# Optimization experiments

Hardware: AMD Instinct MI355X
Metric: run time of the kernel (lower is better)

The kernel has to match this reference:

```python
import math
import jax, jax.numpy as jnp
from jax import lax
import numpy as np

SCORE_THR = 0.5
IOU_THR = 0.7
MIN_SIZE = 1.0
BBOX_CLIP = math.log(1000.0 / 16.0)

FEAT_SIZES = [100, 50, 25, 13, 7]
STRIDES = [8, 16, 32, 64, 128]
RATIOS = (0.5, 1.0, 2.0)
C = 256
A = 3
N = 2


def _make_priors(fs, stride):
    base = stride * 4.0
    ys, xs = np.meshgrid(np.arange(fs), np.arange(fs), indexing='ij')
    cx = (xs + 0.5) * stride
    cy = (ys + 0.5) * stride
    pri = []
    for r in RATIOS:
        w = base / np.sqrt(r)
        h = base * np.sqrt(r)
        pri.append(np.stack([cx - w / 2, cy - h / 2, cx + w / 2, cy + h / 2], axis=-1))
    pri = np.stack(pri, axis=2)  # (fs, fs, A, 4): H,W,A order matches permute/reshape
    return jnp.asarray(pri.reshape(-1, 4), dtype=jnp.float32)


def setup_inputs():
    key = jax.random.key(0)
    ks = jax.random.split(key, 8)
    inp = {}
    for i, fs in enumerate(FEAT_SIZES):
        inp[f'fmap{i}'] = jax.random.normal(jax.random.fold_in(ks[0], i), (N, C, fs, fs), dtype=jnp.float32)
        inp[f'priors{i}'] = _make_priors(fs, STRIDES[i])
    sc = 0.02
    inp['conv_w'] = jax.random.normal(ks[1], (C, C, 3, 3), jnp.float32) * sc
    inp['conv_b'] = jnp.zeros((C,), jnp.float32)
    inp['log_w'] = jax.random.normal(ks[2], (A, C, 1, 1), jnp.float32) * sc
    inp['log_b'] = jnp.zeros((A,), jnp.float32)
    inp['reg_w'] = jax.random.normal(ks[3], (A * 4, C, 1, 1), jnp.float32) * sc
    inp['reg_b'] = jnp.zeros((A * 4,), jnp.float32)
    inp['imsizes'] = jnp.full((N, 2), 800, dtype=jnp.int32)  # (h, w) per image
    inp['lvtop'] = 500
    inp['imtop'] = 100
    return inp


def _conv(x, w, b, pad):
    y = lax.conv_general_dilated(x, w, (1, 1), pad, dimension_numbers=('NCHW', 'OIHW', 'NCHW'))
    return y + b[None, :, None, None]


def _decode(reg, pri):
    pw = pri[..., 2] - pri[..., 0]
    ph = pri[..., 3] - pri[..., 1]
    pcx = pri[..., 0] + 0.5 * pw
    pcy = pri[..., 1] + 0.5 * ph
    dx, dy = reg[..., 0], reg[..., 1]
    dw = jnp.minimum(reg[..., 2], BBOX_CLIP)
    dh = jnp.minimum(reg[..., 3], BBOX_CLIP)
    cx = dx * pw + pcx
    cy = dy * ph + pcy
    w = jnp.exp(dw) * pw
    h = jnp.exp(dh) * ph
    return jnp.stack([cx - 0.5 * w, cy - 0.5 * h, cx + 0.5 * w, cy + 0.5 * h], axis=-1)


def _head(x, priors, conv_w, conv_b, log_w, log_b, reg_w, reg_b, lvtop):
    n = x.shape[0]
    h = jax.nn.relu(_conv(x, conv_w, conv_b, 'SAME'))
    reg = _conv(h, reg_w, reg_b, 'VALID').transpose(0, 2, 3, 1).reshape(n, -1, 4)
    log = _conv(h, log_w, log_b, 'VALID').transpose(0, 2, 3, 1).reshape(n, -1)
    k = min(lvtop, log.shape[1])
    vals, top = lax.top_k(log, k)                           # (n, k)
    reg = jnp.take_along_axis(reg, top[..., None], axis=1)  # (n, k, 4)
    pri = priors[top]                                       # (n, k, 4)
    return _decode(reg, pri), vals, k


def _box_iou(a, b):
    area_a = (a[:, 2] - a[:, 0]) * (a[:, 3] - a[:, 1])
    area_b = (b[:, 2] - b[:, 0]) * (b[:, 3] - b[:, 1])
    lt = jnp.maximum(a[:, None, :2], b[None, :, :2])
    rb = jnp.minimum(a[:, None, 2:], b[None, :, 2:])
    wh = jnp.clip(rb - lt, 0.0)
    inter = wh[..., 0] * wh[..., 1]
    return inter / (area_a[:, None] + area_b[None, :] - inter + 1e-9)


def _forward(fmaps, priors, conv_w, conv_b, log_w, log_b, reg_w, reg_b, imsizes, lvtop, imtop):
    tups = [_head(x, p, conv_w, conv_b, log_w, log_b, reg_w, reg_b, lvtop)
            for x, p in zip(fmaps, priors)]
    boxes = jnp.concatenate([t[0] for t in tups], axis=1)                 # (n, D, 4)
    obj = jax.nn.sigmoid(jnp.concatenate([t[1] for t in tups], axis=1))   # (n, D)
    lvlen = jnp.asarray([t[2] for t in tups])
    n, D = obj.shape
    boxes = boxes.reshape(-1, 4)
    obj = obj.reshape(-1)
    K = n * D
    imidx = jnp.arange(K) // D
    valid = obj >= SCORE_THR                                # score filter (masked, not nonzero)
    hw = imsizes[imidx].astype(jnp.float32)                 # (K, 2) = (h, w)
    x1 = jnp.clip(boxes[:, 0], 0.0, hw[:, 1])
    y1 = jnp.clip(boxes[:, 1], 0.0, hw[:, 0])
    x2 = jnp.clip(boxes[:, 2], 0.0, hw[:, 1])
    y2 = jnp.clip(boxes[:, 3], 0.0, hw[:, 0])
    boxes = jnp.stack([x1, y1, x2, y2], axis=-1)
    valid &= (x2 - x1 >= MIN_SIZE) & (y2 - y1 >= MIN_SIZE)  # remove_small
    lvidx = jnp.searchsorted(jnp.cumsum(lvlen), jnp.arange(K) % D, side='right')
    groups = imidx * 10 + lvidx
    scores = jnp.where(valid, obj, -jnp.inf)
    order = jnp.argsort(-scores)                            # global score order; groups gate suppression
    b, g, v, ii = boxes[order], groups[order], valid[order], imidx[order]
    iou = _box_iou(b, b)                                    # (K, K)
    ar = jnp.arange(K)
    def body(i, keep):
        sup = (iou[i] > IOU_THR) & (g == g[i]) & (ar > i)
        return jnp.where(keep[i], keep & ~sup, keep)
    keep = lax.fori_loop(0, K, body, v)                     # greedy batched NMS
    def select(i):
        m = keep & (ii == i)
        sel = jnp.argsort(~m)[:imtop]                       # stable: kept boxes in score order
        val = m[sel]
        bx = jnp.where(val[:, None], b[sel], 0.0)
        ix = jnp.where(val, i, -1)
        return bx, ix
    bx, ix = jax.vmap(select)(jnp.arange(n))
    return bx.reshape(n * imtop, 4), ix.reshape(n * imtop)


def reference(fmap0, fmap1, fmap2, fmap3, fmap4, priors0, priors1, priors2, priors3, priors4,
              conv_w, conv_b, log_w, log_b, reg_w, reg_b, imsizes, lvtop, imtop):
    return _forward([fmap0, fmap1, fmap2, fmap3, fmap4],
                    [priors0, priors1, priors2, priors3, priors4],
                    conv_w, conv_b, log_w, log_b, reg_w, reg_b, imsizes, lvtop, imtop)
```

## Files before the change

kernel.cpp:

```cpp
#include <hip/hip_runtime.h>
#include <math.h>


#define N_IMG 2
#define C_CH  256
#define D_PER 2147
#define K_TOT 4294
#define K_PAD 8192

__constant__ int c_Ml[5]     = {30000, 7500, 1875, 507, 147};
__constant__ int c_kl[5]     = {500, 500, 500, 500, 147};
__constant__ int c_lvoff[5]  = {0, 500, 1000, 1500, 2000};
__constant__ int c_logoff[5] = {0, 60000, 75000, 78750, 79764};
__constant__ int c_regoff[5] = {0, 240000, 300000, 315000, 319056};
__constant__ int c_fs[5]     = {100, 50, 25, 13, 7};
__constant__ int c_npt[5]    = {13, 7, 4, 2, 1};
__constant__ int c_E[5]      = {10000, 2500, 625, 169, 49};
__constant__ int c_cumbl[6]  = {0, 1352, 1744, 1872, 1904, 1912};
__constant__ int c_hcum[6]   = {0, 157, 197, 207, 210, 211};
__constant__ size_t c_hoff[5] = {0, 5120000, 6400000, 6720000, 6806528};

__global__ void transpose_w_kernel(const float* __restrict__ w,
                                   double* __restrict__ wT2) {
  int i = blockIdx.x * 256 + threadIdx.x;
  if (i >= 589824) return;
  int q = i % 4608;
  int slab = i / 4608;
  int cobi = slab >> 5, ch = slab & 31;
  int ci = q / 576;
  int rem = q % 576;
  int tap = rem / 64, co = rem & 63;
  wT2[i] = (double)w[(size_t)(cobi * 64 + co) * 2304 + (ch * 8 + ci) * 9 + tap];
}

template <typename T>
__global__ __launch_bounds__(256) void conv_fused_kernel(
    const float* __restrict__ x0, const float* __restrict__ x1,
    const float* __restrict__ x2, const float* __restrict__ x3,
    const float* __restrict__ x4, const double* __restrict__ wT2,
    const float* __restrict__ bias, T* __restrict__ h) {
  __shared__ double s_in[8][120];
  __shared__ double s_w[4608];
  int tid = threadIdx.x;
  int bid = blockIdx.x;
  int l = 0;
  while (bid >= c_cumbl[l + 1]) ++l;
  int r = bid - c_cumbl[l];
  int fs = c_fs[l], npt = c_npt[l];
  int tiles = npt * npt;
  int tile = r % tiles;
  int cn = r / tiles;
  int cobi = cn & 3, n = cn >> 2;
  int ptx = tile % npt, pty = tile / npt;
  int px0 = ptx * 8, py0 = pty * 8;
  int E = fs * fs;
  const float* xl;
  switch (l) {
    case 0: xl = x0; break;
    case 1: xl = x1; break;
    case 2: xl = x2; break;
    case 3: xl = x3; break;
    default: xl = x4; break;
  }
  const float* xn = xl + (size_t)n * C_CH * E;
  T* hl = h + c_hoff[l];

  int tpx = tid & 15, tco = tid >> 4;
  int prow = tpx >> 1, pcol0 = (tpx & 1) * 4;

  double acc[4][4];
#pragma unroll
  for (int i = 0; i < 4; i++)
#pragma unroll
    for (int j = 0; j < 4; j++) acc[i][j] = 0.0;

  for (int ch = 0; ch < 32; ++ch) {
    for (int idx = tid; idx < 800; idx += 256) {
      int ci = idx / 100, rr2 = idx % 100;
      int hy = rr2 / 10, hx = rr2 % 10;
      int gy = py0 - 1 + hy, gx = px0 - 1 + hx;
      float v = 0.f;
      if (gy >= 0 && gy < fs && gx >= 0 && gx < fs)
        v = xn[(size_t)(ch * 8 + ci) * E + gy * fs + gx];
      s_in[ci][hy * 12 + hx] = (double)v;
    }
    {
      const double2* src =
          (const double2*)(wT2 + (size_t)(cobi * 32 + ch) * 4608);
      double2* dst = (double2*)s_w;
#pragma unroll
      for (int k = 0; k < 9; k++) {
        int idx = tid + k * 256;
        if (idx < 2304) dst[idx] = src[idx];
      }
    }
    __syncthreads();
#pragma unroll
    for (int ci = 0; ci < 8; ++ci) {
      const double* inp = &s_in[ci][0];
      const double* wpb = &s_w[ci * 576];
#pragma unroll
      for (int ky = 0; ky < 3; ++ky) {
        const double* ip = inp + (prow + ky) * 12 + pcol0;
        double2 a0 = *(const double2*)ip;
        double2 a1 = *(const double2*)(ip + 2);
        double2 a2 = *(const double2*)(ip + 4);
        double d6[6];
        d6[0] = a0.x; d6[1] = a0.y; d6[2] = a1.x;
        d6[3] = a1.y; d6[4] = a2.x; d6[5] = a2.y;
#pragma unroll
        for (int kx = 0; kx < 3; ++kx) {
          const double* wp = wpb + (ky * 3 + kx) * 64 + tco * 4;
          double2 wA = *(const double2*)wp;
          double2 wB = *(const double2*)(wp + 2);
          double w0 = wA.x, w1 = wA.y, w2 = wB.x, w3 = wB.y;
#pragma unroll
          for (int pj = 0; pj < 4; pj++) {
            double iv = d6[pj + kx];
            acc[0][pj] = fma(w0, iv, acc[0][pj]);
            acc[1][pj] = fma(w1, iv, acc[1][pj]);
            acc[2][pj] = fma(w2, iv, acc[2][pj]);
            acc[3][pj] = fma(w3, iv, acc[3][pj]);
          }
        }
      }
    }
    __syncthreads();
  }

  int gy = py0 + prow;
  if (gy < fs) {
#pragma unroll
    for (int coi = 0; coi < 4; ++coi) {
      int co = cobi * 64 + tco * 4 + coi;
      double bb = (double)bias[co];
#pragma unroll
      for (int pj = 0; pj < 4; pj++) {
        int gx = px0 + pcol0 + pj;
        if (gx < fs) {
          double v = acc[coi][pj] + bb;
          hl[((size_t)n * C_CH + co) * E + gy * fs + gx] = (T)fmax(v, 0.0);
        }
      }
    }
  }
}

template <typename T>
__global__ __launch_bounds__(256) void heads_fused_kernel(
    const T* __restrict__ h, const float* __restrict__ logw,
    const float* __restrict__ logb, const float* __restrict__ regw,
    const float* __restrict__ regb, double* __restrict__ logits,
    double* __restrict__ regs) {
  __shared__ float s_wh[256][16];
  __shared__ double s_red[4][15][64];
  int tid = threadIdx.x;
  int n = blockIdx.y;
  int cidx = blockIdx.x;
  int l = 0;
  while (cidx >= c_hcum[l + 1]) ++l;
  int chunk = cidx - c_hcum[l];
  int E = c_E[l];
  int px0 = chunk * 64;
  const T* hl = h + c_hoff[l];
  double* logits_l = logits + c_logoff[l];
  double* regs_l = regs + c_regoff[l];

  for (int idx = tid; idx < 4096; idx += 256) {
    int c = idx >> 4, j = idx & 15;
    float v = 0.f;
    if (j < 3) v = logw[j * 256 + c];
    else if (j < 15) v = regw[(j - 3) * 256 + c];
    s_wh[c][j] = v;
  }
  __syncthreads();

  int p = tid & 63, c4 = tid >> 6;
  int pix = px0 + p;
  bool act = pix < E;
  double acc[15];
#pragma unroll
  for (int j = 0; j < 15; j++) acc[j] = 0.0;
  if (act) {
    const T* hp = hl + ((size_t)n * C_CH + c4 * 64) * E + pix;
    for (int cc = 0; cc < 64; ++cc) {
      double hv = (double)hp[(size_t)cc * E];
      const float* wr = &s_wh[c4 * 64 + cc][0];
#pragma unroll
      for (int j = 0; j < 15; j++)
        acc[j] = fma((double)wr[j], hv, acc[j]);
    }
  }
#pragma unroll
  for (int j = 0; j < 15; j++) s_red[c4][j][p] = acc[j];
  __syncthreads();
  if (act) {
    int M = E * 3;
    for (int j = c4; j < 15; j += 4) {
      double v = s_red[0][j][p] + s_red[1][j][p] + s_red[2][j][p] +
                 s_red[3][j][p];
      if (j < 3) {
        logits_l[(size_t)n * M + pix * 3 + j] = v + (double)logb[j];
      } else {
        int rj = j - 3, a = rj >> 2, coord = rj & 3;
        regs_l[((size_t)n * M + pix * 3 + a) * 4 + coord] =
            v + (double)regb[rj];
      }
    }
  }
}

__device__ __forceinline__ unsigned long long d2key(double v) {
  unsigned long long ub = (unsigned long long)__double_as_longlong(v);
  return (ub >> 63) ? ~ub : (ub | 0x8000000000000000ull);
}

#define TK_CH 30
__global__ __launch_bounds__(1024) void topk_kernel(
    const double* __restrict__ logits, int* __restrict__ cand_anchor) {
  int bid = blockIdx.x;
  int n = bid / 5, l = bid % 5;
  int M = c_Ml[l], k = c_kl[l];
  const double* lg = logits + c_logoff[l] + (size_t)n * M;
  int tid = threadIdx.x;
  __shared__ int histw[16][256];
  __shared__ int hist[256];
  __shared__ unsigned long long s_prefix;
  __shared__ int s_r;
  if (tid == 0) { s_prefix = 0ull; s_r = k; }

  int chunk = (M + 1023) >> 10;
  int i0 = tid * chunk, i1 = min(M, i0 + chunk);
  int cnt = i1 - i0;
  if (cnt < 0) cnt = 0;
  unsigned long long kv[TK_CH];
#pragma unroll
  for (int q = 0; q < TK_CH; q++)
    if (q < cnt) kv[q] = d2key(lg[i0 + q]);
  int wid = tid >> 6;
  __syncthreads();

  for (int pass = 0; pass < 8; ++pass) {
    int shift = 56 - pass * 8;
    for (int i = tid; i < 4096; i += 1024) ((int*)histw)[i] = 0;
    __syncthreads();
    unsigned long long pfx = s_prefix;
    int rr = s_r;
#pragma unroll
    for (int q = 0; q < TK_CH; q++) {
      if (q < cnt) {
        unsigned long long u = kv[q];
        if (pass == 0 || (u >> (shift + 8)) == pfx)
          atomicAdd(&histw[wid][(int)((u >> shift) & 255ull)], 1);
      }
    }
    __syncthreads();
    if (tid < 256) {
      int s = 0;
#pragma unroll
      for (int w = 0; w < 16; w++) s += histw[w][tid];
      hist[tid] = s;
    }
    __syncthreads();
    if (tid == 0) {
      int s = 0, beta = 0;
      for (int b = 255; b >= 0; --b) {
        if (s + hist[b] >= rr) { beta = b; break; }
        s += hist[b];
      }
      s_prefix = (pfx << 8) | (unsigned long long)beta;
      s_r = rr - s;
    }
    __syncthreads();
  }
  unsigned long long T = s_prefix;
  int need = s_r;
  int cgt = 0, ceq = 0;
#pragma unroll
  for (int q = 0; q < TK_CH; q++) {
    if (q < cnt) {
      cgt += (kv[q] > T);
      ceq += (kv[q] == T);
    }
  }
  __shared__ int sgt[1024], seq[1024];
  sgt[tid] = cgt;
  seq[tid] = ceq;
  __syncthreads();
  for (int o = 1; o < 1024; o <<= 1) {
    int a = (tid >= o) ? sgt[tid - o] : 0;
    int b2 = (tid >= o) ? seq[tid - o] : 0;
    __syncthreads();
    sgt[tid] += a;
    seq[tid] += b2;
    __syncthreads();
  }
  int gt_total = sgt[1023];
  int pg = sgt[tid] - cgt, pe = seq[tid] - ceq;
  int base = n * D_PER + c_lvoff[l];
#pragma unroll
  for (int q = 0; q < TK_CH; q++) {
    if (q < cnt) {
      unsigned long long u = kv[q];
      if (u > T) {
        cand_anchor[base + (pg++)] = i0 + q;
      } else if (u == T) {
        if (pe < need) cand_anchor[base + gt_total + pe] = i0 + q;
        pe++;
      }
    }
  }
}

__global__ __launch_bounds__(256) void decode_kernel(
    const int* __restrict__ cand_anchor, const double* __restrict__ logits,
    const double* __restrict__ regs, const float* __restrict__ p0,
    const float* __restrict__ p1, const float* __restrict__ p2,
    const float* __restrict__ p3, const float* __restrict__ p4,
    const int* __restrict__ imsizes, double* __restrict__ cand_score,
    double* __restrict__ cand_box, int* __restrict__ cand_group,
    int* __restrict__ cand_valid) {
  int s = blockIdx.x * 256 + threadIdx.x;
  if (s >= K_TOT) return;
  int n = s / D_PER;
  int rr = s % D_PER;
  int l = (rr < 2000) ? (rr / 500) : 4;
  int aidx = cand_anchor[s];
  int M = c_Ml[l];
  const float* pp;
  switch (l) {
    case 0: pp = p0; break;
    case 1: pp = p1; break;
    case 2: pp = p2; break;
    case 3: pp = p3; break;
    default: pp = p4; break;
  }
  double lv = logits[c_logoff[l] + (size_t)n * M + aidx];
  double obj = 1.0 / (1.0 + exp(-lv));
  const double* rp = regs + c_regoff[l] + ((size_t)n * M + aidx) * 4;
  const float* pr = pp + (size_t)aidx * 4;
  double px1 = pr[0], py1 = pr[1], px2 = pr[2], py2 = pr[3];
  double pw = px2 - px1, ph = py2 - py1;
  double pcx = px1 + 0.5 * pw, pcy = py1 + 0.5 * ph;
  const double BCLIP = 4.1351665567423560;
  double dx = rp[0], dy = rp[1];
  double dw = fmin(rp[2], BCLIP), dh = fmin(rp[3], BCLIP);
  double cx = dx * pw + pcx, cy = dy * ph + pcy;
  double w = exp(dw) * pw, hh = exp(dh) * ph;
  double x1 = cx - 0.5 * w, y1 = cy - 0.5 * hh;
  double x2 = cx + 0.5 * w, y2 = cy + 0.5 * hh;
  double imh = (double)imsizes[n * 2 + 0], imw = (double)imsizes[n * 2 + 1];
  x1 = fmin(fmax(x1, 0.0), imw);
  x2 = fmin(fmax(x2, 0.0), imw);
  y1 = fmin(fmax(y1, 0.0), imh);
  y2 = fmin(fmax(y2, 0.0), imh);
  bool valid = (obj >= 0.5) && ((x2 - x1) >= 1.0) && ((y2 - y1) >= 1.0);
  cand_box[(size_t)s * 4 + 0] = x1;
  cand_box[(size_t)s * 4 + 1] = y1;
  cand_box[(size_t)s * 4 + 2] = x2;
  cand_box[(size_t)s * 4 + 3] = y2;
  cand_score[s] = valid ? obj : -(double)INFINITY;
  cand_group[s] = n * 5 + l;
  cand_valid[s] = valid ? 1 : 0;
}

__global__ __launch_bounds__(1024) void sort_kernel(
    const double* __restrict__ cand_score, int* __restrict__ order) {
  __shared__ unsigned long long key[K_PAD];
  int tid = threadIdx.x;
  for (int i = tid; i < K_PAD; i += 1024) {
    unsigned long long kk = 0ull;
    if (i < K_TOT) {
      unsigned long long u = d2key(cand_score[i]);
      kk = (u & ~0x1FFFull) | (unsigned long long)i;
    }
    key[i] = kk;
  }
  __syncthreads();
  for (int k = 2; k <= K_PAD; k <<= 1) {
    for (int j = k >> 1; j > 0; j >>= 1) {
      for (int i = tid; i < K_PAD; i += 1024) {
        int ixj = i ^ j;
        if (ixj > i) {
          unsigned long long a = key[i], b = key[ixj];
          bool sw = ((i & k) == 0) ? (a < b) : (a > b);
          if (sw) { key[i] = b; key[ixj] = a; }
        }
      }
      __syncthreads();
    }
  }
  for (int i = tid; i < K_TOT; i += 1024)
    order[i] = (int)(key[i] & 0x1FFFull);
}

__global__ __launch_bounds__(256) void gather_kernel(
    const int* __restrict__ order, const double* __restrict__ cand_box,
    const int* __restrict__ cand_group, const int* __restrict__ cand_valid,
    double* __restrict__ box_s, int* __restrict__ grp_s,
    int* __restrict__ img_s, int* __restrict__ valid_s,
    int* __restrict__ keep_s) {
  int i = blockIdx.x * 256 + threadIdx.x;
  if (i >= K_TOT) return;
  int s = order[i];
#pragma unroll
  for (int q = 0; q < 4; q++)
    box_s[(size_t)i * 4 + q] = cand_box[(size_t)s * 4 + q];
  int g = cand_group[s];
  grp_s[i] = g;
  img_s[i] = g / 5;
  valid_s[i] = cand_valid[s];
  keep_s[i] = 0;
}

#define MAXM 512
__global__ __launch_bounds__(256) void nms_kernel(
    const double* __restrict__ box_s, const int* __restrict__ grp_s,
    const int* __restrict__ valid_s, int* __restrict__ keep_s) {
  int g = blockIdx.x;
  int tid = threadIdx.x;
  __shared__ int cnt[256];
  __shared__ int mem[MAXM];
  __shared__ double bx[MAXM][4];
  __shared__ unsigned long long mask[MAXM][8];
  const int chunk = (K_TOT + 255) / 256;
  int i0 = tid * chunk, i1 = min(K_TOT, i0 + chunk);
  int c = 0;
  for (int i = i0; i < i1; ++i) c += (grp_s[i] == g && valid_s[i]);
  cnt[tid] = c;
  __syncthreads();
  for (int o = 1; o < 256; o <<= 1) {
    int v = (tid >= o) ? cnt[tid - o] : 0;
    __syncthreads();
    cnt[tid] += v;
    __syncthreads();
  }
  int off = cnt[tid] - c;
  int m = cnt[255];
  for (int i = i0; i < i1; ++i)
    if (grp_s[i] == g && valid_s[i]) mem[off++] = i;
  __syncthreads();
  for (int t = tid; t < m; t += 256) {
    int i = mem[t];
#pragma unroll
    for (int q = 0; q < 4; q++) bx[t][q] = box_s[(size_t)i * 4 + q];
  }
  __syncthreads();
  for (int i = tid; i < m; i += 256) {
    unsigned long long row[8] = {0, 0, 0, 0, 0, 0, 0, 0};
    double ax1 = bx[i][0], ay1 = bx[i][1], ax2 = bx[i][2], ay2 = bx[i][3];
    double areaA = (ax2 - ax1) * (ay2 - ay1);
    for (int j = i + 1; j < m; ++j) {
      double bx1 = bx[j][0], by1 = bx[j][1], bx2 = bx[j][2], by2 = bx[j][3];
      double areaB = (bx2 - bx1) * (by2 - by1);
      double lx = fmax(ax1, bx1), ly = fmax(ay1, by1);
      double rx = fmin(ax2, bx2), ry = fmin(ay2, by2);
      double iw = fmax(rx - lx, 0.0), ih = fmax(ry - ly, 0.0);
      double inter = iw * ih;
      double iou = inter / (areaA + areaB - inter + 1e-9);
      if (iou > 0.7) row[j >> 6] |= (1ull << (j & 63));
    }
#pragma unroll
    for (int w2 = 0; w2 < 8; ++w2) mask[i][w2] = row[w2];
  }
  __syncthreads();
  if (tid == 0) {
    unsigned long long remv[8] = {0, 0, 0, 0, 0, 0, 0, 0};
    for (int i = 0; i < m; ++i) {
      if (!((remv[i >> 6] >> (i & 63)) & 1ull)) {
        keep_s[mem[i]] = 1;
#pragma unroll
        for (int w2 = 0; w2 < 8; ++w2) remv[w2] |= mask[i][w2];
      }
    }
  }
}

__global__ __launch_bounds__(256) void select_kernel(
    const double* __restrict__ box_s, const int* __restrict__ img_s,
    const int* __restrict__ keep_s, float* __restrict__ out) {
  int n = blockIdx.x;
  int tid = threadIdx.x;
  __shared__ int cnt[256];
  const int chunk = (K_TOT + 255) / 256;
  int i0 = tid * chunk, i1 = min(K_TOT, i0 + chunk);
  int c = 0;
  for (int i = i0; i < i1; ++i) c += (keep_s[i] && img_s[i] == n);
  cnt[tid] = c;
  __syncthreads();
  for (int o = 1; o < 256; o <<= 1) {
    int v = (tid >= o) ? cnt[tid - o] : 0;
    __syncthreads();
    cnt[tid] += v;
    __syncthreads();
  }
  int pos = cnt[tid] - c;
  int total = cnt[255];
  for (int i = i0; i < i1; ++i) {
    if (keep_s[i] && img_s[i] == n) {
      if (pos < 100) {
#pragma unroll
        for (int q = 0; q < 4; q++)
          out[(n * 100 + pos) * 4 + q] = (float)box_s[(size_t)i * 4 + q];
        out[800 + n * 100 + pos] = (float)n;
      }
      pos++;
    }
  }
  for (int p = total + tid; p < 100; p += 256) {
#pragma unroll
    for (int q = 0; q < 4; q++) out[(n * 100 + p) * 4 + q] = 0.0f;
    out[800 + n * 100 + p] = -1.0f;
  }
}

extern "C" void kernel_launch(void* const* d_in, const int* in_sizes, int n_in,
                              void* d_out, int out_size, void* d_ws,
                              size_t ws_size, hipStream_t stream) {
  (void)in_sizes; (void)n_in; (void)out_size;
  const float* fmap[5];
  const float* priors[5];
  for (int l = 0; l < 5; l++) {
    fmap[l] = (const float*)d_in[2 * l];
    priors[l] = (const float*)d_in[2 * l + 1];
  }
  const float* conv_w = (const float*)d_in[10];
  const float* conv_b = (const float*)d_in[11];
  const float* log_w = (const float*)d_in[12];
  const float* log_b = (const float*)d_in[13];
  const float* reg_w = (const float*)d_in[14];
  const float* reg_b = (const float*)d_in[15];
  const int* imsizes = (const int*)d_in[16];
  float* out = (float*)d_out;

  bool f64h = ws_size >= (size_t)66000000;

  char* base = (char*)d_ws;
  size_t off = 0;
  auto alloc = [&](size_t bytes) -> void* {
    off = (off + 255) & ~(size_t)255;
    void* p = base + off;
    off += bytes;
    return p;
  };
  double* wT2 = (double*)alloc(589824ull * 8);
  void* hraw = alloc(6831616ull * (f64h ? 8 : 4));
  double* logits = (double*)alloc(80058ull * 8);
  double* regs = (double*)alloc(320232ull * 8);
  int* cand_anchor = (int*)alloc(K_TOT * 4);
  double* cand_score = (double*)alloc(K_TOT * 8);
  double* cand_box = (double*)alloc((size_t)K_TOT * 4 * 8);
  int* cand_group = (int*)alloc(K_TOT * 4);
  int* cand_valid = (int*)alloc(K_TOT * 4);
  int* order = (int*)alloc(K_TOT * 4);
  double* box_s = (double*)alloc((size_t)K_TOT * 4 * 8);
  int* grp_s = (int*)alloc(K_TOT * 4);
  int* img_s = (int*)alloc(K_TOT * 4);
  int* valid_s = (int*)alloc(K_TOT * 4);
  int* keep_s = (int*)alloc(K_TOT * 4);

  transpose_w_kernel<<<2304, 256, 0, stream>>>(conv_w, wT2);

  if (f64h) {
    conv_fused_kernel<double><<<1912, 256, 0, stream>>>(
        fmap[0], fmap[1], fmap[2], fmap[3], fmap[4], wT2, conv_b,
        (double*)hraw);
    heads_fused_kernel<double><<<dim3(211, 2), 256, 0, stream>>>(
        (double*)hraw, log_w, log_b, reg_w, reg_b, logits, regs);
  } else {
    conv_fused_kernel<float><<<1912, 256, 0, stream>>>(
        fmap[0], fmap[1], fmap[2], fmap[3], fmap[4], wT2, conv_b,
        (float*)hraw);
    heads_fused_kernel<float><<<dim3(211, 2), 256, 0, stream>>>(
        (float*)hraw, log_w, log_b, reg_w, reg_b, logits, regs);
  }
  topk_kernel<<<10, 1024, 0, stream>>>(logits, cand_anchor);
  decode_kernel<<<(K_TOT + 255) / 256, 256, 0, stream>>>(
      cand_anchor, logits, regs, priors[0], priors[1], priors[2], priors[3],
      priors[4], imsizes, cand_score, cand_box, cand_group, cand_valid);
  sort_kernel<<<1, 1024, 0, stream>>>(cand_score, order);
  gather_kernel<<<(K_TOT + 255) / 256, 256, 0, stream>>>(
      order, cand_box, cand_group, cand_valid, box_s, grp_s, img_s, valid_s,
      keep_s);
  nms_kernel<<<10, 256, 0, stream>>>(box_s, grp_s, valid_s, keep_s);
  select_kernel<<<2, 256, 0, stream>>>(box_s, img_s, keep_s, out);
}
```

Before: 1.239 ms.

## Restructure conv to wave-uniform weight loads and fuse topk/decode, sort/gather

The conv kernel drops the shared-memory weight tile. Each wave now owns 16 output channels and reads weights directly from global memory with wave-uniform addresses, and each lane computes one pixel. Input staging indices are precomputed once, and block IDs are swizzled across the XCDs. Separately, topk is fused with decode through a shared selection list, and sort is fused with gather, which removes two launches and the intermediate buffers. The risks are reduced per-thread register reuse in the conv (one pixel per thread), more global/scalar load traffic, and dependence on the weight fetches being cached.

```diff
diff --git a/kernel.cpp b/kernel.cpp
--- a/kernel.cpp
+++ b/kernel.cpp
@@ -7,6 +7,8 @@
 #define D_PER 2147
 #define K_TOT 4294
 #define K_PAD 8192
+#define CONV_BLOCKS 1912
+#define CPX 239
 
 __constant__ int c_Ml[5]     = {30000, 7500, 1875, 507, 147};
 __constant__ int c_kl[5]     = {500, 500, 500, 500, 147};
@@ -30,7 +32,8 @@
   int ci = q / 576;
   int rem = q % 576;
   int tap = rem / 64, co = rem & 63;
-  wT2[i] = (double)w[(size_t)(cobi * 64 + co) * 2304 + (ch * 8 + ci) * 9 + tap];
+  wT2[i] =
+      (double)w[(size_t)(cobi * 64 + co) * 2304 + (ch * 8 + ci) * 9 + tap];
 }
 
 template <typename T>
@@ -39,10 +42,9 @@
     const float* __restrict__ x2, const float* __restrict__ x3,
     const float* __restrict__ x4, const double* __restrict__ wT2,
     const float* __restrict__ bias, T* __restrict__ h) {
-  __shared__ double s_in[8][120];
-  __shared__ double s_w[4608];
+  __shared__ double s_in[8 * 120];
   int tid = threadIdx.x;
-  int bid = blockIdx.x;
+  int bid = (blockIdx.x & 7) * CPX + (blockIdx.x >> 3);
   int l = 0;
   while (bid >= c_cumbl[l + 1]) ++l;
   int r = bid - c_cumbl[l];
@@ -65,83 +67,72 @@
   const float* xn = xl + (size_t)n * C_CH * E;
   T* hl = h + c_hoff[l];
 
-  int tpx = tid & 15, tco = tid >> 4;
-  int prow = tpx >> 1, pcol0 = (tpx & 1) * 4;
-
-  double acc[4][4];
-#pragma unroll
-  for (int i = 0; i < 4; i++)
-#pragma unroll
-    for (int j = 0; j < 4; j++) acc[i][j] = 0.0;
-
-  for (int ch = 0; ch < 32; ++ch) {
-    for (int idx = tid; idx < 800; idx += 256) {
+  int lane = tid & 63;
+  int wvu = __builtin_amdgcn_readfirstlane(tid >> 6);
+  int prow = lane >> 3, pcol = lane & 7;
+
+  int in_dst[4], in_src[4];
+#pragma unroll
+  for (int it = 0; it < 4; ++it) {
+    int idx = tid + it * 256;
+    in_dst[it] = -1;
+    in_src[it] = -1;
+    if (idx < 800) {
       int ci = idx / 100, rr2 = idx % 100;
       int hy = rr2 / 10, hx = rr2 % 10;
       int gy = py0 - 1 + hy, gx = px0 - 1 + hx;
-      float v = 0.f;
+      in_dst[it] = ci * 120 + hy * 12 + hx;
       if (gy >= 0 && gy < fs && gx >= 0 && gx < fs)
-        v = xn[(size_t)(ch * 8 + ci) * E + gy * fs + gx];
-      s_in[ci][hy * 12 + hx] = (double)v;
-    }
-    {
-      const double2* src =
-          (const double2*)(wT2 + (size_t)(cobi * 32 + ch) * 4608);
-      double2* dst = (double2*)s_w;
-#pragma unroll
-      for (int k = 0; k < 9; k++) {
-        int idx = tid + k * 256;
-        if (idx < 2304) dst[idx] = src[idx];
-      }
-    }
-    __syncthreads();
+        in_src[it] = ci * E + gy * fs + gx;
+    }
+  }
+
+  double acc[16];
+#pragma unroll
+  for (int c = 0; c < 16; ++c) acc[c] = 0.0;
+
+  const double* __restrict__ wbase =
+      wT2 + (size_t)(cobi * 32) * 4608 + wvu * 16;
+
+  for (int ch = 0; ch < 32; ++ch) {
+    const float* xc = xn + (size_t)(ch * 8) * E;
+#pragma unroll
+    for (int it = 0; it < 4; ++it) {
+      if (in_dst[it] >= 0)
+        s_in[in_dst[it]] = (in_src[it] >= 0) ? (double)xc[in_src[it]] : 0.0;
+    }
+    __syncthreads();
+    const double* __restrict__ wch = wbase + (size_t)ch * 4608;
 #pragma unroll
     for (int ci = 0; ci < 8; ++ci) {
-      const double* inp = &s_in[ci][0];
-      const double* wpb = &s_w[ci * 576];
+      const double* inp = &s_in[ci * 120];
 #pragma unroll
       for (int ky = 0; ky < 3; ++ky) {
-        const double* ip = inp + (prow + ky) * 12 + pcol0;
-        double2 a0 = *(const double2*)ip;
-        double2 a1 = *(const double2*)(ip + 2);
-        double2 a2 = *(const double2*)(ip + 4);
-        double d6[6];
-        d6[0] = a0.x; d6[1] = a0.y; d6[2] = a1.x;
-        d6[3] = a1.y; d6[4] = a2.x; d6[5] = a2.y;
+        const double* ip = inp + (prow + ky) * 12 + pcol;
+        double iv[3];
+        iv[0] = ip[0];
+        iv[1] = ip[1];
+        iv[2] = ip[2];
 #pragma unroll
         for (int kx = 0; kx < 3; ++kx) {
-          const double* wp = wpb + (ky * 3 + kx) * 64 + tco * 4;
-          double2 wA = *(const double2*)wp;
-          double2 wB = *(const double2*)(wp + 2);
-          double w0 = wA.x, w1 = wA.y, w2 = wB.x, w3 = wB.y;
-#pragma unroll
-          for (int pj = 0; pj < 4; pj++) {
-            double iv = d6[pj + kx];
-            acc[0][pj] = fma(w0, iv, acc[0][pj]);
-            acc[1][pj] = fma(w1, iv, acc[1][pj]);
-            acc[2][pj] = fma(w2, iv, acc[2][pj]);
-            acc[3][pj] = fma(w3, iv, acc[3][pj]);
-          }
+          const double* __restrict__ wk = wch + (ci * 9 + ky * 3 + kx) * 64;
+          double ivx = iv[kx];
+#pragma unroll
+          for (int c = 0; c < 16; ++c)
+            acc[c] = fma(wk[c], ivx, acc[c]);
         }
       }
     }
     __syncthreads();
   }
 
-  int gy = py0 + prow;
-  if (gy < fs) {
-#pragma unroll
-    for (int coi = 0; coi < 4; ++coi) {
-      int co = cobi * 64 + tco * 4 + coi;
-      double bb = (double)bias[co];
-#pragma unroll
-      for (int pj = 0; pj < 4; pj++) {
-        int gx = px0 + pcol0 + pj;
-        if (gx < fs) {
-          double v = acc[coi][pj] + bb;
-          hl[((size_t)n * C_CH + co) * E + gy * fs + gx] = (T)fmax(v, 0.0);
-        }
-      }
+  int gy = py0 + prow, gx = px0 + pcol;
+  if (gy < fs && gx < fs) {
+#pragma unroll
+    for (int c = 0; c < 16; ++c) {
+      int co = cobi * 64 + wvu * 16 + c;
+      double v = acc[c] + (double)bias[co];
+      hl[((size_t)n * C_CH + co) * E + gy * fs + gx] = (T)fmax(v, 0.0);
     }
   }
 }
@@ -216,8 +207,13 @@
 }
 
 #define TK_CH 30
-__global__ __launch_bounds__(1024) void topk_kernel(
-    const double* __restrict__ logits, int* __restrict__ cand_anchor) {
+__global__ __launch_bounds__(1024) void topk_decode_kernel(
+    const double* __restrict__ logits, const double* __restrict__ regs,
+    const float* __restrict__ p0, const float* __restrict__ p1,
+    const float* __restrict__ p2, const float* __restrict__ p3,
+    const float* __restrict__ p4, const int* __restrict__ imsizes,
+    double* __restrict__ cand_score, double* __restrict__ cand_box,
+    int* __restrict__ cand_group, int* __restrict__ cand_valid) {
   int bid = blockIdx.x;
   int n = bid / 5, l = bid % 5;
   int M = c_Ml[l], k = c_kl[l];
@@ -225,6 +221,7 @@
   int tid = threadIdx.x;
   __shared__ int histw[16][256];
   __shared__ int hist[256];
+  __shared__ int s_sel[512];
   __shared__ unsigned long long s_prefix;
   __shared__ int s_r;
   if (tid == 0) { s_prefix = 0ull; s_r = k; }
@@ -297,36 +294,20 @@
   }
   int gt_total = sgt[1023];
   int pg = sgt[tid] - cgt, pe = seq[tid] - ceq;
-  int base = n * D_PER + c_lvoff[l];
 #pragma unroll
   for (int q = 0; q < TK_CH; q++) {
     if (q < cnt) {
       unsigned long long u = kv[q];
       if (u > T) {
-        cand_anchor[base + (pg++)] = i0 + q;
+        s_sel[pg++] = i0 + q;
       } else if (u == T) {
-        if (pe < need) cand_anchor[base + gt_total + pe] = i0 + q;
+        if (pe < need) s_sel[gt_total + pe] = i0 + q;
         pe++;
       }
     }
   }
-}
-
-__global__ __launch_bounds__(256) void decode_kernel(
-    const int* __restrict__ cand_anchor, const double* __restrict__ logits,
-    const double* __restrict__ regs, const float* __restrict__ p0,
-    const float* __restrict__ p1, const float* __restrict__ p2,
-    const float* __restrict__ p3, const float* __restrict__ p4,
-    const int* __restrict__ imsizes, double* __restrict__ cand_score,
-    double* __restrict__ cand_box, int* __restrict__ cand_group,
-    int* __restrict__ cand_valid) {
-  int s = blockIdx.x * 256 + threadIdx.x;
-  if (s >= K_TOT) return;
-  int n = s / D_PER;
-  int rr = s % D_PER;
-  int l = (rr < 2000) ? (rr / 500) : 4;
-  int aidx = cand_anchor[s];
-  int M = c_Ml[l];
+  __syncthreads();
+
   const float* pp;
   switch (l) {
     case 0: pp = p0; break;
@@ -335,37 +316,46 @@
     case 3: pp = p3; break;
     default: pp = p4; break;
   }
-  double lv = logits[c_logoff[l] + (size_t)n * M + aidx];
-  double obj = 1.0 / (1.0 + exp(-lv));
-  const double* rp = regs + c_regoff[l] + ((size_t)n * M + aidx) * 4;
-  const float* pr = pp + (size_t)aidx * 4;
-  double px1 = pr[0], py1 = pr[1], px2 = pr[2], py2 = pr[3];
-  double pw = px2 - px1, ph = py2 - py1;
-  double pcx = px1 + 0.5 * pw, pcy = py1 + 0.5 * ph;
+  const double* regs_l = regs + c_regoff[l];
+  double imh = (double)imsizes[n * 2 + 0], imw = (double)imsizes[n * 2 + 1];
   const double BCLIP = 4.1351665567423560;
-  double dx = rp[0], dy = rp[1];
-  double dw = fmin(rp[2], BCLIP), dh = fmin(rp[3], BCLIP);
-  double cx = dx * pw + pcx, cy = dy * ph + pcy;
-  double w = exp(dw) * pw, hh = exp(dh) * ph;
-  double x1 = cx - 0.5 * w, y1 = cy - 0.5 * hh;
-  double x2 = cx + 0.5 * w, y2 = cy + 0.5 * hh;
-  double imh = (double)imsizes[n * 2 + 0], imw = (double)imsizes[n * 2 + 1];
-  x1 = fmin(fmax(x1, 0.0), imw);
-  x2 = fmin(fmax(x2, 0.0), imw);
-  y1 = fmin(fmax(y1, 0.0), imh);
-  y2 = fmin(fmax(y2, 0.0), imh);
-  bool valid = (obj >= 0.5) && ((x2 - x1) >= 1.0) && ((y2 - y1) >= 1.0);
-  cand_box[(size_t)s * 4 + 0] = x1;
-  cand_box[(size_t)s * 4 + 1] = y1;
-  cand_box[(size_t)s * 4 + 2] = x2;
-  cand_box[(size_t)s * 4 + 3] = y2;
-  cand_score[s] = valid ? obj : -(double)INFINITY;
-  cand_group[s] = n * 5 + l;
-  cand_valid[s] = valid ? 1 : 0;
-}
-
-__global__ __launch_bounds__(1024) void sort_kernel(
-    const double* __restrict__ cand_score, int* __restrict__ order) {
+  for (int i = tid; i < k; i += 1024) {
+    int aidx = s_sel[i];
+    int slot = n * D_PER + c_lvoff[l] + i;
+    double lv = lg[aidx];
+    double obj = 1.0 / (1.0 + exp(-lv));
+    const double* rp = regs_l + ((size_t)n * M + aidx) * 4;
+    const float* pr = pp + (size_t)aidx * 4;
+    double px1 = pr[0], py1 = pr[1], px2 = pr[2], py2 = pr[3];
+    double pw = px2 - px1, ph = py2 - py1;
+    double pcx = px1 + 0.5 * pw, pcy = py1 + 0.5 * ph;
+    double dx = rp[0], dy = rp[1];
+    double dw = fmin(rp[2], BCLIP), dh = fmin(rp[3], BCLIP);
+    double cx = dx * pw + pcx, cy = dy * ph + pcy;
+    double w = exp(dw) * pw, hh = exp(dh) * ph;
+    double x1 = cx - 0.5 * w, y1 = cy - 0.5 * hh;
+    double x2 = cx + 0.5 * w, y2 = cy + 0.5 * hh;
+    x1 = fmin(fmax(x1, 0.0), imw);
+    x2 = fmin(fmax(x2, 0.0), imw);
+    y1 = fmin(fmax(y1, 0.0), imh);
+    y2 = fmin(fmax(y2, 0.0), imh);
+    bool valid = (obj >= 0.5) && ((x2 - x1) >= 1.0) && ((y2 - y1) >= 1.0);
+    cand_box[(size_t)slot * 4 + 0] = x1;
+    cand_box[(size_t)slot * 4 + 1] = y1;
+    cand_box[(size_t)slot * 4 + 2] = x2;
+    cand_box[(size_t)slot * 4 + 3] = y2;
+    cand_score[slot] = valid ? obj : -(double)INFINITY;
+    cand_group[slot] = n * 5 + l;
+    cand_valid[slot] = valid ? 1 : 0;
+  }
+}
+
+__global__ __launch_bounds__(1024) void sort_gather_kernel(
+    const double* __restrict__ cand_score, const double* __restrict__ cand_box,
+    const int* __restrict__ cand_group, const int* __restrict__ cand_valid,
+    double* __restrict__ box_s, int* __restrict__ grp_s,
+    int* __restrict__ img_s, int* __restrict__ valid_s,
+    int* __restrict__ keep_s) {
   __shared__ unsigned long long key[K_PAD];
   int tid = threadIdx.x;
   for (int i = tid; i < K_PAD; i += 1024) {
@@ -390,27 +380,17 @@
       __syncthreads();
     }
   }
-  for (int i = tid; i < K_TOT; i += 1024)
-    order[i] = (int)(key[i] & 0x1FFFull);
-}
-
-__global__ __launch_bounds__(256) void gather_kernel(
-    const int* __restrict__ order, const double* __restrict__ cand_box,
-    const int* __restrict__ cand_group, const int* __restrict__ cand_valid,
-    double* __restrict__ box_s, int* __restrict__ grp_s,
-    int* __restrict__ img_s, int* __restrict__ valid_s,
-    int* __restrict__ keep_s) {
-  int i = blockIdx.x * 256 + threadIdx.x;
-  if (i >= K_TOT) return;
-  int s = order[i];
-#pragma unroll
-  for (int q = 0; q < 4; q++)
-    box_s[(size_t)i * 4 + q] = cand_box[(size_t)s * 4 + q];
-  int g = cand_group[s];
-  grp_s[i] = g;
-  img_s[i] = g / 5;
-  valid_s[i] = cand_valid[s];
-  keep_s[i] = 0;
+  for (int i = tid; i < K_TOT; i += 1024) {
+    int s = (int)(key[i] & 0x1FFFull);
+#pragma unroll
+    for (int q = 0; q < 4; q++)
+      box_s[(size_t)i * 4 + q] = cand_box[(size_t)s * 4 + q];
+    int g = cand_group[s];
+    grp_s[i] = g;
+    img_s[i] = g / 5;
+    valid_s[i] = cand_valid[s];
+    keep_s[i] = 0;
+  }
 }
 
 #define MAXM 512
@@ -547,12 +527,10 @@
   void* hraw = alloc(6831616ull * (f64h ? 8 : 4));
   double* logits = (double*)alloc(80058ull * 8);
   double* regs = (double*)alloc(320232ull * 8);
-  int* cand_anchor = (int*)alloc(K_TOT * 4);
   double* cand_score = (double*)alloc(K_TOT * 8);
   double* cand_box = (double*)alloc((size_t)K_TOT * 4 * 8);
   int* cand_group = (int*)alloc(K_TOT * 4);
   int* cand_valid = (int*)alloc(K_TOT * 4);
-  int* order = (int*)alloc(K_TOT * 4);
   double* box_s = (double*)alloc((size_t)K_TOT * 4 * 8);
   int* grp_s = (int*)alloc(K_TOT * 4);
   int* img_s = (int*)alloc(K_TOT * 4);
@@ -562,26 +540,24 @@
   transpose_w_kernel<<<2304, 256, 0, stream>>>(conv_w, wT2);
 
   if (f64h) {
-    conv_fused_kernel<double><<<1912, 256, 0, stream>>>(
+    conv_fused_kernel<double><<<CONV_BLOCKS, 256, 0, stream>>>(
         fmap[0], fmap[1], fmap[2], fmap[3], fmap[4], wT2, conv_b,
         (double*)hraw);
     heads_fused_kernel<double><<<dim3(211, 2), 256, 0, stream>>>(
         (double*)hraw, log_w, log_b, reg_w, reg_b, logits, regs);
   } else {
-    conv_fused_kernel<float><<<1912, 256, 0, stream>>>(
+    conv_fused_kernel<float><<<CONV_BLOCKS, 256, 0, stream>>>(
         fmap[0], fmap[1], fmap[2], fmap[3], fmap[4], wT2, conv_b,
         (float*)hraw);
     heads_fused_kernel<float><<<dim3(211, 2), 256, 0, stream>>>(
         (float*)hraw, log_w, log_b, reg_w, reg_b, logits, regs);
   }
-  topk_kernel<<<10, 1024, 0, stream>>>(logits, cand_anchor);
-  decode_kernel<<<(K_TOT + 255) / 256, 256, 0, stream>>>(
-      cand_anchor, logits, regs, priors[0], priors[1], priors[2], priors[3],
-      priors[4], imsizes, cand_score, cand_box, cand_group, cand_valid);
-  sort_kernel<<<1, 1024, 0, stream>>>(cand_score, order);
-  gather_kernel<<<(K_TOT + 255) / 256, 256, 0, stream>>>(
-      order, cand_box, cand_group, cand_valid, box_s, grp_s, img_s, valid_s,
-      keep_s);
+  topk_decode_kernel<<<10, 1024, 0, stream>>>(
+      logits, regs, priors[0], priors[1], priors[2], priors[3], priors[4],
+      imsizes, cand_score, cand_box, cand_group, cand_valid);
+  sort_gather_kernel<<<1, 1024, 0, stream>>>(
+      cand_score, cand_box, cand_group, cand_valid, box_s, grp_s, img_s,
+      valid_s, keep_s);
   nms_kernel<<<10, 256, 0, stream>>>(box_s, grp_s, valid_s, keep_s);
   select_kernel<<<2, 256, 0, stream>>>(box_s, img_s, keep_s, out);
 }
```

Result: slower. 1.660 ms (+34.0%).
